# Performance work log

Hardware: AMD Instinct MI355X
Metric: run time of the kernel (lower is better)

Reference implementation:

```python
import jax, jax.numpy as jnp
import numpy as np

HIDDEN = 768
ENT = 9
D = 64  # inner_dim
BIG = 1e12


def _rope_tables(seq_len, dim):
    # layout after torch stack([sin,cos],-1).reshape: [sin0,cos0,sin1,cos1,...]
    pos = jnp.arange(seq_len, dtype=jnp.float32)[:, None]          # [S,1]
    inv = jnp.power(10000.0, -2.0 * jnp.arange(dim // 2, dtype=jnp.float32) / dim)
    ang = pos * inv                                                 # [S,D/2]
    # repeat_interleave(2): [c0,c0,c1,c1,...]
    cos = jnp.repeat(jnp.cos(ang), 2, axis=-1)[:, None, :]          # [S,1,D]
    sin = jnp.repeat(jnp.sin(ang), 2, axis=-1)[:, None, :]
    return sin, cos


def _rotate_half_interleaved(x):
    # stack([-x_odd, x_even], -1).reshape -> [-x1, x0, -x3, x2, ...]
    return jnp.stack([-x[..., 1::2], x[..., ::2]], axis=-1).reshape(x.shape)


def _multilabel_ce(logits, labels):
    # standard GlobalPointer multilabel categorical crossentropy
    B = logits.shape[0]
    y_pred = logits.reshape(B * ENT, -1)
    y_true = labels.reshape(B * ENT, -1)
    y_pred = (1.0 - 2.0 * y_true) * y_pred
    y_neg = y_pred - y_true * BIG
    y_pos = y_pred - (1.0 - y_true) * BIG
    neg = jnp.logaddexp(0.0, jax.scipy.special.logsumexp(y_neg, axis=-1))
    pos = jnp.logaddexp(0.0, jax.scipy.special.logsumexp(y_pos, axis=-1))
    return jnp.mean(neg + pos)


def setup_inputs() -> dict:
    key = jax.random.key(0)
    k1, k2, k3, k4 = jax.random.split(key, 4)
    B, S = 16, 512
    last_hidden_state = jax.random.normal(k1, (B, S, HIDDEN), dtype=jnp.float32)
    attention_mask = jnp.ones((B, S), dtype=jnp.int32)
    batch_labels = jax.random.randint(k2, (B, ENT, S, S), 0, 2).astype(jnp.int32)
    W = jax.random.normal(k3, (HIDDEN, ENT * D * 2), dtype=jnp.float32) * 0.02
    b = jnp.zeros((ENT * D * 2,), dtype=jnp.float32)
    return {"last_hidden_state": last_hidden_state, "attention_mask": attention_mask,
            "batch_labels": batch_labels, "W": W, "b": b}


def reference(last_hidden_state, attention_mask, batch_labels, W, b):
    B, S, _ = last_hidden_state.shape
    out = last_hidden_state @ W + b                     # [B,S,ENT*2D]
    out = out.reshape(B, S, ENT, 2 * D)
    qw, kw = out[..., :D], out[..., D:]                 # [B,S,ENT,D]

    sin, cos = _rope_tables(S, D)                       # [S,1,D]
    qw = qw * cos + _rotate_half_interleaved(qw) * sin
    kw = kw * cos + _rotate_half_interleaved(kw) * sin

    logits = jnp.einsum('bmhd,bnhd->bhmn', qw, kw)      # [B,ENT,S,S]

    pad = attention_mask.astype(jnp.float32)[:, None, None, :]  # mask over key dim n
    logits = logits * pad - (1.0 - pad) * BIG
    tril = jnp.tril(jnp.ones((S, S), dtype=jnp.float32), -1)
    logits = logits - tril * BIG
    temp_logits = logits / (D ** 0.5)

    loss = _multilabel_ce(temp_logits, batch_labels.astype(jnp.float32))
    return loss, temp_logits
```

## Files before the change

kernel.cpp:

```cpp
#include <hip/hip_runtime.h>
#include <hip/hip_bf16.h>

#define HID 768
#define ENTS 9
#define DD 64
#define NOUT 1152
#define BATCH 16
#define SEQ 512
#define BIGF 1000000000000.0f
#define BIG8 125000000000.0f
#define NCHUNK 16

typedef __attribute__((ext_vector_type(8))) short short8;
typedef __attribute__((ext_vector_type(4))) short short4_t;
typedef __attribute__((ext_vector_type(4))) float floatx4;
typedef __attribute__((ext_vector_type(2))) float floatx2;
typedef __attribute__((ext_vector_type(4))) int intx4;
typedef unsigned short ushort_t;

static __device__ __forceinline__ ushort_t f2bf(float x) {
    unsigned int u = __float_as_uint(x);
    unsigned int r = (u + 0x7FFFu + ((u >> 16) & 1u)) >> 16;
    return (ushort_t)r;
}

static __device__ __forceinline__ void gload16(const void* g, void* l) {
    __builtin_amdgcn_global_load_lds(
        (const __attribute__((address_space(1))) void*)g,
        (__attribute__((address_space(3))) void*)l, 16, 0, 0);
}

__global__ __launch_bounds__(256) void prep_kernel(
    const float* __restrict__ X, const float* __restrict__ W,
    float* __restrict__ sin_t, float* __restrict__ cos_t,
    ushort_t* __restrict__ Xb, ushort_t* __restrict__ Wt)
{
    const int tid = blockIdx.x * 256 + threadIdx.x;
    const int nth = gridDim.x * 256;

    for (int idx = tid; idx < SEQ * 32; idx += nth) {
        int m = idx >> 5, i = idx & 31;
        float inv = powf(10000.0f, -2.0f * (float)i / 64.0f);
        float ang = (float)m * inv;
        sin_t[idx] = sinf(ang);
        cos_t[idx] = cosf(ang);
    }
    for (int idx = tid; idx < NOUT * HID; idx += nth) {
        int n = idx / HID, k = idx - n * HID;
        Wt[idx] = f2bf(W[(size_t)k * NOUT + n]);
    }
    const int nx4 = BATCH * SEQ * HID / 4;
    for (int idx = tid; idx < nx4; idx += nth) {
        float4 f = *(const float4*)&X[idx * 4];
        ushort_t* p = &Xb[idx * 4];
        p[0] = f2bf(f.x); p[1] = f2bf(f.y); p[2] = f2bf(f.z); p[3] = f2bf(f.w);
    }
}

__global__ __launch_bounds__(256) void proj_rope_kernel(
    const ushort_t* __restrict__ Xb, const ushort_t* __restrict__ Wt,
    const float* __restrict__ bias,
    const float* __restrict__ sin_t, const float* __restrict__ cos_t,
    ushort_t* __restrict__ qbuf, ushort_t* __restrict__ kbuf)
{
    __shared__ ushort_t As[128 * 32];
    __shared__ ushort_t Bs[128 * 32];
    const int tid  = threadIdx.x;
    const int lane = tid & 63;
    const int wave = tid >> 6;
    const int bm = blockIdx.x * 128;
    const int bn = blockIdx.y * 128;
    const int wm = (wave >> 1) * 64;
    const int wn = (wave & 1) * 64;

    floatx4 acc[4][4];
    #pragma unroll
    for (int j = 0; j < 4; ++j)
        #pragma unroll
        for (int i = 0; i < 4; ++i) { floatx4 z = {0.f,0.f,0.f,0.f}; acc[j][i] = z; }

    const int c0 = wave * 64 + lane;
    const int c1 = 256 + wave * 64 + lane;
    const int r0 = c0 >> 2, q0 = (c0 & 3) * 8;
    const int r1 = c1 >> 2, q1 = (c1 & 3) * 8;
    ushort_t* ldsA0 = As + wave * 512;
    ushort_t* ldsA1 = As + 2048 + wave * 512;
    ushort_t* ldsB0 = Bs + wave * 512;
    ushort_t* ldsB1 = Bs + 2048 + wave * 512;

    const int ko = (lane >> 4) * 8;
    const int lr = lane & 15;

    for (int kt = 0; kt < HID; kt += 32) {
        gload16(&Xb[(size_t)(bm + r0) * HID + kt + q0], ldsA0);
        gload16(&Xb[(size_t)(bm + r1) * HID + kt + q1], ldsA1);
        gload16(&Wt[(size_t)(bn + r0) * HID + kt + q0], ldsB0);
        gload16(&Wt[(size_t)(bn + r1) * HID + kt + q1], ldsB1);
        __syncthreads();

        short8 a[4], b[4];
        #pragma unroll
        for (int i = 0; i < 4; ++i) a[i] = *(const short8*)&As[(wm + i*16 + lr) * 32 + ko];
        #pragma unroll
        for (int j = 0; j < 4; ++j) b[j] = *(const short8*)&Bs[(wn + j*16 + lr) * 32 + ko];
        #pragma unroll
        for (int j = 0; j < 4; ++j)
            #pragma unroll
            for (int i = 0; i < 4; ++i)
                acc[j][i] = __builtin_amdgcn_mfma_f32_16x16x32_bf16(b[j], a[i], acc[j][i], 0, 0, 0);
        __syncthreads();
    }

    #pragma unroll
    for (int j = 0; j < 4; ++j) {
        const int n0 = bn + wn + j*16 + (lane >> 4) * 4;
        const int e   = n0 >> 7;
        const int dd0 = n0 & 127;
        const bool isq = dd0 < DD;
        const int d0  = isq ? dd0 : dd0 - DD;
        const float4 bv = *(const float4*)&bias[n0];
        #pragma unroll
        for (int i = 0; i < 4; ++i) {
            const int m = bm + wm + i*16 + lr;
            const int s  = m & (SEQ - 1);
            const int bb = m >> 9;
            const float c0f = cos_t[s*32 + (d0 >> 1)];
            const float s0f = sin_t[s*32 + (d0 >> 1)];
            const float c1f = cos_t[s*32 + (d0 >> 1) + 1];
            const float s1f = sin_t[s*32 + (d0 >> 1) + 1];
            const float v0 = acc[j][i][0] + bv.x;
            const float v1 = acc[j][i][1] + bv.y;
            const float v2 = acc[j][i][2] + bv.z;
            const float v3 = acc[j][i][3] + bv.w;
            const float o0 = v0 * c0f - v1 * s0f;
            const float o1 = v1 * c0f + v0 * s0f;
            const float o2 = v2 * c1f - v3 * s1f;
            const float o3 = v3 * c1f + v2 * s1f;
            short4_t sv = { (short)f2bf(o0), (short)f2bf(o1), (short)f2bf(o2), (short)f2bf(o3) };
            size_t oidx = (((size_t)(bb * ENTS + e) * SEQ) + s) * DD + d0;
            *(short4_t*)&(isq ? qbuf : kbuf)[oidx] = sv;
        }
    }
}

__global__ __launch_bounds__(256) void qk_mask_ce_kernel(
    const ushort_t* __restrict__ qbuf, const ushort_t* __restrict__ kbuf,
    const int* __restrict__ amask, const int* __restrict__ labels,
    float* __restrict__ logits, float* __restrict__ partials)
{
    __shared__ ushort_t Qs[128][72];
    __shared__ ushort_t Ks[128][72];
    __shared__ float ssn[4], ssp[4];
    const int tid  = threadIdx.x;

    const int wrk = (blockIdx.x & 7) * 288 + (blockIdx.x >> 3);
    const int bh = wrk >> 4;
    const int xy = wrk & 15;
    const int bx = xy >> 2, by = xy & 3;
    const int bm = bx * 128;
    const int bn = by * 128;
    const int b  = bh / ENTS;
    const int bhbase = bh << 18;

    if (bx > by) {
        const int c4 = (tid & 31) << 2;
        const int rr = tid >> 5;

        const intx4 pf = *(const intx4*)&amask[(b << 9) + bn + c4];
        floatx4 cv;
        #pragma unroll
        for (int e = 0; e < 4; ++e) cv[e] = (float)pf[e] * BIG8 - 2.0f * BIG8;
        float cvm1 = 0.f;
        if (c4 > 0) {
            const int pfm1 = amask[(b << 9) + bn + c4 - 1];
            cvm1 = (float)pfm1 * BIG8 - 2.0f * BIG8;
        }
        const floatx4 sh = { cvm1, cv.x, cv.y, cv.z };
        const floatx2 h2 = { cv.y, cv.z };

        int cnt = 0;
        for (int pass = 0; pass < 16; ++pass) {
            const int m = bm + pass * 8 + rr;
            const int off = bhbase + (m << 9) + bn + c4;
            const intx4 y4 = *(const intx4*)&labels[off];
            #pragma unroll
            for (int e = 0; e < 4; ++e) cnt += (y4[e] & 1) & pf[e];
            if (c4 == 0) {
                logits[off] = cv.x;
                *(floatx2*)&logits[off + 1] = h2;
            } else {
                *(floatx4*)&logits[off - 1] = sh;
            }
            if (c4 == 124) logits[off + 3] = cv.w;
        }

        #pragma unroll
        for (int o = 32; o > 0; o >>= 1) cnt += __shfl_down(cnt, o);
        if ((tid & 63) == 0) ssn[tid >> 6] = (float)cnt;
        __syncthreads();
        if (tid == 0) {
            float SP = ssn[0] + ssn[1] + ssn[2] + ssn[3];
            floatx2 res = { 0.f, SP };
            *(floatx2*)&partials[(size_t)(bh * NCHUNK + xy) * 2] = res;
        }
        return;
    }

    const int lane = tid & 63;
    const int wave = tid >> 6;
    const int wm = (wave >> 1) * 64;
    const int wn = (wave & 1) * 64;
    const size_t base = (size_t)bh * SEQ * DD;

    const int g  = lane >> 4;
    const int lr = lane & 15;
    const int ko = g * 8;
    const int r0 = bm + wm + lr;
    const int W  = bn + wn;
    const int n00 = W + (g << 2);

    const bool diag = (bx == by);

    intx4 yc[2][4];
    #pragma unroll
    for (int jh = 0; jh < 2; ++jh)
        #pragma unroll
        for (int i = 0; i < 4; ++i)
            yc[jh][i] = *(const intx4*)&labels[bhbase + ((r0 + i*16) << 9) + n00 + jh*16];

    floatx4 pm8[4], pc[4];
    #pragma unroll
    for (int j = 0; j < 4; ++j) {
        const intx4 p4 = *(const intx4*)&amask[(b << 9) + n00 + j*16];
        #pragma unroll
        for (int rg = 0; rg < 4; ++rg) {
            const float pf = (float)p4[rg];
            pm8[j][rg] = pf * 0.125f;
            pc[j][rg]  = (pf - 1.0f) * BIG8;
        }
    }

    {
        const int r  = tid >> 1;
        const int ks = (tid & 1) * 32;
        const ushort_t* gq = &qbuf[base + (size_t)(bm + r) * DD + ks];
        const ushort_t* gk = &kbuf[base + (size_t)(bn + r) * DD + ks];
        #pragma unroll
        for (int uu = 0; uu < 4; ++uu) {
            *(short8*)&Qs[r][ks + uu*8] = *(const short8*)(gq + uu*8);
            *(short8*)&Ks[r][ks + uu*8] = *(const short8*)(gk + uu*8);
        }
    }
    __syncthreads();

    short8 a[2][4];
    #pragma unroll
    for (int kk = 0; kk < 2; ++kk)
        #pragma unroll
        for (int i = 0; i < 4; ++i)
            a[kk][i] = *(const short8*)&Qs[wm + i*16 + lr][kk*32 + ko];

    float smn = 0.f, smp = 0.f;
    float tl[4];
    float* __restrict__ lgb = logits + bhbase;

    #pragma unroll
    for (int jp = 0; jp < 2; ++jp) {
        const int jA = jp * 2, jB = jp * 2 + 1;

        floatx4 accA[4], accB[4];
        #pragma unroll
        for (int i = 0; i < 4; ++i) { floatx4 z = {0.f,0.f,0.f,0.f}; accA[i] = z; accB[i] = z; }
        #pragma unroll
        for (int kk = 0; kk < 2; ++kk) {
            const short8 bfA = *(const short8*)&Ks[wn + jA*16 + lr][kk*32 + ko];
            const short8 bfB = *(const short8*)&Ks[wn + jB*16 + lr][kk*32 + ko];
            #pragma unroll
            for (int i = 0; i < 4; ++i) {
                accA[i] = __builtin_amdgcn_mfma_f32_16x16x32_bf16(bfA, a[kk][i], accA[i], 0, 0, 0);
                accB[i] = __builtin_amdgcn_mfma_f32_16x16x32_bf16(bfB, a[kk][i], accB[i], 0, 0, 0);
            }
        }

        unsigned int yb = 0;
        {
            int cnt = 0;
            #pragma unroll
            for (int jh = 0; jh < 2; ++jh)
                #pragma unroll
                for (int i = 0; i < 4; ++i)
                    #pragma unroll
                    for (int rg = 0; rg < 4; ++rg) {
                        yb |= (unsigned)(yc[jh][i][rg] & 1) << cnt;
                        ++cnt;
                    }
        }

        if (jp == 0) {
            #pragma unroll
            for (int jh = 0; jh < 2; ++jh)
                #pragma unroll
                for (int i = 0; i < 4; ++i)
                    yc[jh][i] = *(const intx4*)&labels[bhbase + ((r0 + i*16) << 9) + n00 + (2 + jh)*16];
        }

        int cnt = 0;
        #pragma unroll
        for (int half = 0; half < 2; ++half) {
            const int j = half ? jB : jA;
            const floatx4 pm = pm8[j], pcj = pc[j];
            const int n0j = W + j*16 + (g << 2);
            #pragma unroll
            for (int i = 0; i < 4; ++i) {
                const int m = r0 + i*16;
                const int d = m - n0j;
                floatx4 v = half ? accB[i] : accA[i];
                #pragma unroll
                for (int rg = 0; rg < 4; ++rg) {
                    float t = fmaf(v[rg], pm[rg], pcj[rg]);
                    if (diag && (d > rg)) t -= BIG8;
                    v[rg] = t;
                    const int yy = (int)((yb >> cnt) & 1u);
                    const float uu = __uint_as_float(__float_as_uint(t) ^ ((unsigned)yy << 31));
                    const float cN = yy ? -BIGF : 0.0f;
                    const float cP = yy ? -BIG8 : -BIGF;
                    smn += __expf(uu + cN);
                    smp += __expf(uu + cP);
                    ++cnt;
                }
                if (half) accB[i] = v; else accA[i] = v;
            }
        }

        #pragma unroll
        for (int i = 0; i < 4; ++i) {
            const floatx4 vA = accA[i], vB = accB[i];
            const int m = r0 + i*16;
            float* __restrict__ row = lgb + (m << 9);
            const float sameA  = __shfl(vA.w, (lane - 16) & 63);
            const float tailA  = __shfl(tl[i], lr + 48);
            const float sameB  = __shfl(vB.w, (lane - 16) & 63);
            const float crossB = __shfl(vA.w, lr + 48);
            const float uA0 = (g == 0) ? tailA  : sameA;
            const float uB0 = (g == 0) ? crossB : sameB;
            if (jp == 0 && g == 0) {
                row[W] = vA.x;
                floatx2 h2 = { vA.y, vA.z };
                *(floatx2*)&row[W + 1] = h2;
            } else {
                floatx4 uA = { uA0, vA.x, vA.y, vA.z };
                *(floatx4*)&row[W + jA*16 + (g << 2) - 1] = uA;
            }
            floatx4 uB = { uB0, vB.x, vB.y, vB.z };
            *(floatx4*)&row[W + jB*16 + (g << 2) - 1] = uB;
            tl[i] = vB.w;
        }
    }

    if (g == 3) {
        #pragma unroll
        for (int i = 0; i < 4; ++i) {
            const int m = r0 + i*16;
            lgb[(m << 9) + W + 63] = tl[i];
        }
    }

    #pragma unroll
    for (int off = 32; off > 0; off >>= 1) {
        smn += __shfl_down(smn, off);
        smp += __shfl_down(smp, off);
    }
    if (lane == 0) { ssn[wave] = smn; ssp[wave] = smp; }
    __syncthreads();
    if (tid == 0) {
        float SN = ssn[0] + ssn[1] + ssn[2] + ssn[3];
        float SP = ssp[0] + ssp[1] + ssp[2] + ssp[3];
        floatx2 res = { SN, SP };
        *(floatx2*)&partials[(size_t)(bh * NCHUNK + xy) * 2] = res;
    }
}

static __device__ __forceinline__ float lae0(float x) {
    return fmaxf(x, 0.f) + log1pf(__expf(-fabsf(x)));
}

__global__ __launch_bounds__(256) void ce_final_kernel(
    const float* __restrict__ partials, float* __restrict__ out)
{
    __shared__ float red[256];
    const int t = threadIdx.x;
    float val = 0.f;
    if (t < BATCH * ENTS) {
        float SN = 0.f, SP = 0.f;
        for (int c = 0; c < NCHUNK; ++c) {
            SN += partials[(size_t)(t * NCHUNK + c) * 2];
            SP += partials[(size_t)(t * NCHUNK + c) * 2 + 1];
        }
        const float neg = log1pf(SN);
        const float pos = lae0(BIG8 + logf(SP));
        val = neg + pos;
    }
    red[t] = val;
    __syncthreads();
    for (int s2 = 128; s2 > 0; s2 >>= 1) {
        if (t < s2) red[t] += red[t + s2];
        __syncthreads();
    }
    if (t == 0) out[0] = red[0] / (float)(BATCH * ENTS);
}

extern "C" void kernel_launch(void* const* d_in, const int* in_sizes, int n_in,
                              void* d_out, int out_size, void* d_ws, size_t ws_size,
                              hipStream_t stream) {
    const float* X      = (const float*)d_in[0];
    const int*   amask  = (const int*)d_in[1];
    const int*   labels = (const int*)d_in[2];
    const float* W      = (const float*)d_in[3];
    const float* bias   = (const float*)d_in[4];

    float* out    = (float*)d_out;
    float* logits = out + 1;

    float* sin_t = (float*)d_ws;
    float* cos_t = sin_t + SEQ * 32;
    ushort_t* Xb   = (ushort_t*)(cos_t + SEQ * 32);
    ushort_t* Wt   = Xb + (size_t)BATCH * SEQ * HID;
    ushort_t* qbuf = Wt + (size_t)NOUT * HID;
    ushort_t* kbuf = qbuf + (size_t)BATCH * ENTS * SEQ * DD;
    float* partials = (float*)(kbuf + (size_t)BATCH * ENTS * SEQ * DD);

    prep_kernel<<<1024, 256, 0, stream>>>(X, W, sin_t, cos_t, Xb, Wt);
    proj_rope_kernel<<<dim3(64, 9), 256, 0, stream>>>(Xb, Wt, bias, sin_t, cos_t, qbuf, kbuf);
    qk_mask_ce_kernel<<<2304, 256, 0, stream>>>(qbuf, kbuf, amask, labels, logits, partials);
    ce_final_kernel<<<1, 256, 0, stream>>>(partials, out);
}
```

Before: 134.2 us.

## Make QK/CE kernel persistent over three tiles with register prefetch of next Q/K

The QK-logits/CE kernel now launches 768 blocks, each processing three consecutive 128x128 tiles. While the current tile computes, the Q/K rows for the next full tile are prefetched into registers and then stored to shared memory at the start of that tile. The work mapping changes from the interleaved blockIdx swizzle to contiguous triples. The per-column mask is now loaded inside the loop instead of being precomputed. This aims to hide global-load latency and amortize launch cost, at the expense of more register pressure (launch_bounds 256,3), an extra barrier per tile, and possibly load imbalance because consecutive tiles mix masked-only and full tiles.

```diff
diff --git a/kernel.cpp b/kernel.cpp
--- a/kernel.cpp
+++ b/kernel.cpp
@@ -143,7 +143,19 @@
     }
 }
 
-__global__ __launch_bounds__(256) void qk_mask_ce_kernel(
+#define IS_FULL(w_) ((((w_) & 15) >> 2) <= (((w_) & 15) & 3))
+#define STAGE(w_) do {                                                          \
+    const int bh_ = (w_) >> 4, xy_ = (w_) & 15;                                 \
+    const size_t base_ = (size_t)bh_ * SEQ * DD;                                \
+    const ushort_t* gq_ = &qbuf[base_ + (size_t)(((xy_ >> 2) * 128) + r) * DD + ks]; \
+    const ushort_t* gk_ = &kbuf[base_ + (size_t)(((xy_ & 3) * 128) + r) * DD + ks];  \
+    S[0] = *(const short8*)(gq_);      S[1] = *(const short8*)(gq_ + 8);        \
+    S[2] = *(const short8*)(gq_ + 16); S[3] = *(const short8*)(gq_ + 24);       \
+    S[4] = *(const short8*)(gk_);      S[5] = *(const short8*)(gk_ + 8);        \
+    S[6] = *(const short8*)(gk_ + 16); S[7] = *(const short8*)(gk_ + 24);       \
+} while (0)
+
+__global__ __launch_bounds__(256, 3) void qk_mask_ce_kernel(
     const ushort_t* __restrict__ qbuf, const ushort_t* __restrict__ kbuf,
     const int* __restrict__ amask, const int* __restrict__ labels,
     float* __restrict__ logits, float* __restrict__ partials)
@@ -152,231 +164,224 @@
     __shared__ ushort_t Ks[128][72];
     __shared__ float ssn[4], ssp[4];
     const int tid  = threadIdx.x;
-
-    const int wrk = (blockIdx.x & 7) * 288 + (blockIdx.x >> 3);
-    const int bh = wrk >> 4;
-    const int xy = wrk & 15;
-    const int bx = xy >> 2, by = xy & 3;
-    const int bm = bx * 128;
-    const int bn = by * 128;
-    const int b  = bh / ENTS;
-    const int bhbase = bh << 18;
-
-    if (bx > by) {
-        const int c4 = (tid & 31) << 2;
-        const int rr = tid >> 5;
-
-        const intx4 pf = *(const intx4*)&amask[(b << 9) + bn + c4];
-        floatx4 cv;
-        #pragma unroll
-        for (int e = 0; e < 4; ++e) cv[e] = (float)pf[e] * BIG8 - 2.0f * BIG8;
-        float cvm1 = 0.f;
-        if (c4 > 0) {
-            const int pfm1 = amask[(b << 9) + bn + c4 - 1];
-            cvm1 = (float)pfm1 * BIG8 - 2.0f * BIG8;
-        }
-        const floatx4 sh = { cvm1, cv.x, cv.y, cv.z };
-        const floatx2 h2 = { cv.y, cv.z };
-
-        int cnt = 0;
-        for (int pass = 0; pass < 16; ++pass) {
-            const int m = bm + pass * 8 + rr;
-            const int off = bhbase + (m << 9) + bn + c4;
-            const intx4 y4 = *(const intx4*)&labels[off];
-            #pragma unroll
-            for (int e = 0; e < 4; ++e) cnt += (y4[e] & 1) & pf[e];
-            if (c4 == 0) {
-                logits[off] = cv.x;
-                *(floatx2*)&logits[off + 1] = h2;
-            } else {
-                *(floatx4*)&logits[off - 1] = sh;
-            }
-            if (c4 == 124) logits[off + 3] = cv.w;
-        }
-
-        #pragma unroll
-        for (int o = 32; o > 0; o >>= 1) cnt += __shfl_down(cnt, o);
-        if ((tid & 63) == 0) ssn[tid >> 6] = (float)cnt;
-        __syncthreads();
-        if (tid == 0) {
-            float SP = ssn[0] + ssn[1] + ssn[2] + ssn[3];
-            floatx2 res = { 0.f, SP };
-            *(floatx2*)&partials[(size_t)(bh * NCHUNK + xy) * 2] = res;
-        }
-        return;
-    }
-
     const int lane = tid & 63;
     const int wave = tid >> 6;
-    const int wm = (wave >> 1) * 64;
-    const int wn = (wave & 1) * 64;
-    const size_t base = (size_t)bh * SEQ * DD;
-
     const int g  = lane >> 4;
     const int lr = lane & 15;
     const int ko = g * 8;
-    const int r0 = bm + wm + lr;
-    const int W  = bn + wn;
-    const int n00 = W + (g << 2);
-
-    const bool diag = (bx == by);
-
-    intx4 yc[2][4];
-    #pragma unroll
-    for (int jh = 0; jh < 2; ++jh)
-        #pragma unroll
-        for (int i = 0; i < 4; ++i)
-            yc[jh][i] = *(const intx4*)&labels[bhbase + ((r0 + i*16) << 9) + n00 + jh*16];
-
-    floatx4 pm8[4], pc[4];
-    #pragma unroll
-    for (int j = 0; j < 4; ++j) {
-        const intx4 p4 = *(const intx4*)&amask[(b << 9) + n00 + j*16];
-        #pragma unroll
-        for (int rg = 0; rg < 4; ++rg) {
-            const float pf = (float)p4[rg];
-            pm8[j][rg] = pf * 0.125f;
-            pc[j][rg]  = (pf - 1.0f) * BIG8;
-        }
-    }
-
-    {
-        const int r  = tid >> 1;
-        const int ks = (tid & 1) * 32;
-        const ushort_t* gq = &qbuf[base + (size_t)(bm + r) * DD + ks];
-        const ushort_t* gk = &kbuf[base + (size_t)(bn + r) * DD + ks];
-        #pragma unroll
-        for (int uu = 0; uu < 4; ++uu) {
-            *(short8*)&Qs[r][ks + uu*8] = *(const short8*)(gq + uu*8);
-            *(short8*)&Ks[r][ks + uu*8] = *(const short8*)(gk + uu*8);
-        }
-    }
-    __syncthreads();
-
-    short8 a[2][4];
-    #pragma unroll
-    for (int kk = 0; kk < 2; ++kk)
-        #pragma unroll
-        for (int i = 0; i < 4; ++i)
-            a[kk][i] = *(const short8*)&Qs[wm + i*16 + lr][kk*32 + ko];
-
-    float smn = 0.f, smp = 0.f;
-    float tl[4];
-    float* __restrict__ lgb = logits + bhbase;
-
-    #pragma unroll
-    for (int jp = 0; jp < 2; ++jp) {
-        const int jA = jp * 2, jB = jp * 2 + 1;
-
-        floatx4 accA[4], accB[4];
-        #pragma unroll
-        for (int i = 0; i < 4; ++i) { floatx4 z = {0.f,0.f,0.f,0.f}; accA[i] = z; accB[i] = z; }
-        #pragma unroll
-        for (int kk = 0; kk < 2; ++kk) {
-            const short8 bfA = *(const short8*)&Ks[wn + jA*16 + lr][kk*32 + ko];
-            const short8 bfB = *(const short8*)&Ks[wn + jB*16 + lr][kk*32 + ko];
-            #pragma unroll
-            for (int i = 0; i < 4; ++i) {
-                accA[i] = __builtin_amdgcn_mfma_f32_16x16x32_bf16(bfA, a[kk][i], accA[i], 0, 0, 0);
-                accB[i] = __builtin_amdgcn_mfma_f32_16x16x32_bf16(bfB, a[kk][i], accB[i], 0, 0, 0);
-            }
-        }
-
-        unsigned int yb = 0;
-        {
+    const int r  = tid >> 1;
+    const int ks = (tid & 1) * 32;
+
+    short8 S[8];
+    const int w0 = blockIdx.x * 3;
+    if (IS_FULL(w0)) STAGE(w0);
+
+    for (int t = 0; t < 3; ++t) {
+        const int w  = w0 + t;
+        const int bh = w >> 4;
+        const int xy = w & 15;
+        const int bx = xy >> 2, by = xy & 3;
+        const int bm = bx * 128, bn = by * 128;
+        const int b  = bh / ENTS;
+        const int bhbase = bh << 18;
+
+        if (t > 0) __syncthreads();
+
+        if (bx > by) {
+            if (t < 2 && IS_FULL(w + 1)) STAGE(w + 1);
+
+            const int c4 = (tid & 31) << 2;
+            const int rr = tid >> 5;
+            const intx4 pf = *(const intx4*)&amask[(b << 9) + bn + c4];
+            floatx4 cv;
+            #pragma unroll
+            for (int e = 0; e < 4; ++e) cv[e] = (float)pf[e] * BIG8 - 2.0f * BIG8;
+            float cvm1 = 0.f;
+            if (c4 > 0) {
+                const int pfm1 = amask[(b << 9) + bn + c4 - 1];
+                cvm1 = (float)pfm1 * BIG8 - 2.0f * BIG8;
+            }
+            const floatx4 sh = { cvm1, cv.x, cv.y, cv.z };
+            const floatx2 h2 = { cv.y, cv.z };
+
             int cnt = 0;
-            #pragma unroll
-            for (int jh = 0; jh < 2; ++jh)
+            for (int pass = 0; pass < 16; ++pass) {
+                const int m = bm + pass * 8 + rr;
+                const int off = bhbase + (m << 9) + bn + c4;
+                const intx4 y4 = *(const intx4*)&labels[off];
                 #pragma unroll
-                for (int i = 0; i < 4; ++i)
+                for (int e = 0; e < 4; ++e) cnt += (y4[e] & 1) & pf[e];
+                if (c4 == 0) {
+                    logits[off] = cv.x;
+                    *(floatx2*)&logits[off + 1] = h2;
+                } else {
+                    *(floatx4*)&logits[off - 1] = sh;
+                }
+                if (c4 == 124) logits[off + 3] = cv.w;
+            }
+
+            #pragma unroll
+            for (int o = 32; o > 0; o >>= 1) cnt += __shfl_down(cnt, o);
+            if ((tid & 63) == 0) ssn[tid >> 6] = (float)cnt;
+            __syncthreads();
+            if (tid == 0) {
+                float SP = ssn[0] + ssn[1] + ssn[2] + ssn[3];
+                floatx2 res = { 0.f, SP };
+                *(floatx2*)&partials[(size_t)(bh * NCHUNK + xy) * 2] = res;
+            }
+            continue;
+        }
+
+        const int wm = (wave >> 1) * 64;
+        const int wn = (wave & 1) * 64;
+        const int r0 = bm + wm + lr;
+        const int W  = bn + wn;
+        const int n00 = W + (g << 2);
+        const bool diag = (bx == by);
+
+        #pragma unroll
+        for (int u = 0; u < 4; ++u) *(short8*)&Qs[r][ks + u*8] = S[u];
+        #pragma unroll
+        for (int u = 0; u < 4; ++u) *(short8*)&Ks[r][ks + u*8] = S[4 + u];
+        __syncthreads();
+
+        intx4 yc[2][4];
+        #pragma unroll
+        for (int jh = 0; jh < 2; ++jh)
+            #pragma unroll
+            for (int i = 0; i < 4; ++i)
+                yc[jh][i] = *(const intx4*)&labels[bhbase + ((r0 + i*16) << 9) + n00 + jh*16];
+
+        short8 a[2][4];
+        #pragma unroll
+        for (int kk = 0; kk < 2; ++kk)
+            #pragma unroll
+            for (int i = 0; i < 4; ++i)
+                a[kk][i] = *(const short8*)&Qs[wm + i*16 + lr][kk*32 + ko];
+
+        if (t < 2 && IS_FULL(w + 1)) STAGE(w + 1);
+
+        float smn = 0.f, smp = 0.f;
+        float tl[4];
+        float* __restrict__ lgb = logits + bhbase;
+
+        #pragma unroll
+        for (int jp = 0; jp < 2; ++jp) {
+            const int jA = jp * 2, jB = jp * 2 + 1;
+
+            floatx4 accA[4], accB[4];
+            #pragma unroll
+            for (int i = 0; i < 4; ++i) { floatx4 z = {0.f,0.f,0.f,0.f}; accA[i] = z; accB[i] = z; }
+            #pragma unroll
+            for (int kk = 0; kk < 2; ++kk) {
+                const short8 bfA = *(const short8*)&Ks[wn + jA*16 + lr][kk*32 + ko];
+                const short8 bfB = *(const short8*)&Ks[wn + jB*16 + lr][kk*32 + ko];
+                #pragma unroll
+                for (int i = 0; i < 4; ++i) {
+                    accA[i] = __builtin_amdgcn_mfma_f32_16x16x32_bf16(bfA, a[kk][i], accA[i], 0, 0, 0);
+                    accB[i] = __builtin_amdgcn_mfma_f32_16x16x32_bf16(bfB, a[kk][i], accB[i], 0, 0, 0);
+                }
+            }
+
+            unsigned int yb = 0;
+            {
+                int cnt = 0;
+                #pragma unroll
+                for (int jh = 0; jh < 2; ++jh)
+                    #pragma unroll
+                    for (int i = 0; i < 4; ++i)
+                        #pragma unroll
+                        for (int rg = 0; rg < 4; ++rg) {
+                            yb |= (unsigned)(yc[jh][i][rg] & 1) << cnt;
+                            ++cnt;
+                        }
+            }
+            if (jp == 0) {
+                #pragma unroll
+                for (int jh = 0; jh < 2; ++jh)
+                    #pragma unroll
+                    for (int i = 0; i < 4; ++i)
+                        yc[jh][i] = *(const intx4*)&labels[bhbase + ((r0 + i*16) << 9) + n00 + (2 + jh)*16];
+            }
+
+            const intx4 p4A = *(const intx4*)&amask[(b << 9) + n00 + jA*16];
+            const intx4 p4B = *(const intx4*)&amask[(b << 9) + n00 + jB*16];
+
+            int cnt = 0;
+            #pragma unroll
+            for (int half = 0; half < 2; ++half) {
+                const int j = half ? jB : jA;
+                const intx4 p4 = half ? p4B : p4A;
+                const int n0j = W + j*16 + (g << 2);
+                #pragma unroll
+                for (int i = 0; i < 4; ++i) {
+                    const int m = r0 + i*16;
+                    const int d = m - n0j;
+                    floatx4 v = half ? accB[i] : accA[i];
                     #pragma unroll
                     for (int rg = 0; rg < 4; ++rg) {
-                        yb |= (unsigned)(yc[jh][i][rg] & 1) << cnt;
+                        const float pf = (float)p4[rg];
+                        float tt = fmaf(v[rg], pf * 0.125f, (pf - 1.0f) * BIG8);
+                        if (diag && (d > rg)) tt -= BIG8;
+                        v[rg] = tt;
+                        const int yy = (int)((yb >> cnt) & 1u);
+                        const float uu = __uint_as_float(__float_as_uint(tt) ^ ((unsigned)yy << 31));
+                        const float cN = yy ? -BIGF : 0.0f;
+                        const float cP = yy ? -BIG8 : -BIGF;
+                        smn += __expf(uu + cN);
+                        smp += __expf(uu + cP);
                         ++cnt;
                     }
-        }
-
-        if (jp == 0) {
-            #pragma unroll
-            for (int jh = 0; jh < 2; ++jh)
-                #pragma unroll
-                for (int i = 0; i < 4; ++i)
-                    yc[jh][i] = *(const intx4*)&labels[bhbase + ((r0 + i*16) << 9) + n00 + (2 + jh)*16];
-        }
-
-        int cnt = 0;
-        #pragma unroll
-        for (int half = 0; half < 2; ++half) {
-            const int j = half ? jB : jA;
-            const floatx4 pm = pm8[j], pcj = pc[j];
-            const int n0j = W + j*16 + (g << 2);
+                    if (half) accB[i] = v; else accA[i] = v;
+                }
+            }
+
+            #pragma unroll
+            for (int i = 0; i < 4; ++i) {
+                const floatx4 vA = accA[i], vB = accB[i];
+                const int m = r0 + i*16;
+                float* __restrict__ row = lgb + (m << 9);
+                const float sameA  = __shfl(vA.w, (lane - 16) & 63);
+                const float tailA  = __shfl(tl[i], lr + 48);
+                const float sameB  = __shfl(vB.w, (lane - 16) & 63);
+                const float crossB = __shfl(vA.w, lr + 48);
+                const float uA0 = (g == 0) ? tailA  : sameA;
+                const float uB0 = (g == 0) ? crossB : sameB;
+                if (jp == 0 && g == 0) {
+                    row[W] = vA.x;
+                    floatx2 h2 = { vA.y, vA.z };
+                    *(floatx2*)&row[W + 1] = h2;
+                } else {
+                    floatx4 uA = { uA0, vA.x, vA.y, vA.z };
+                    *(floatx4*)&row[W + jA*16 + (g << 2) - 1] = uA;
+                }
+                floatx4 uB = { uB0, vB.x, vB.y, vB.z };
+                *(floatx4*)&row[W + jB*16 + (g << 2) - 1] = uB;
+                tl[i] = vB.w;
+            }
+        }
+
+        if (g == 3) {
             #pragma unroll
             for (int i = 0; i < 4; ++i) {
                 const int m = r0 + i*16;
-                const int d = m - n0j;
-                floatx4 v = half ? accB[i] : accA[i];
-                #pragma unroll
-                for (int rg = 0; rg < 4; ++rg) {
-                    float t = fmaf(v[rg], pm[rg], pcj[rg]);
-                    if (diag && (d > rg)) t -= BIG8;
-                    v[rg] = t;
-                    const int yy = (int)((yb >> cnt) & 1u);
-                    const float uu = __uint_as_float(__float_as_uint(t) ^ ((unsigned)yy << 31));
-                    const float cN = yy ? -BIGF : 0.0f;
-                    const float cP = yy ? -BIG8 : -BIGF;
-                    smn += __expf(uu + cN);
-                    smp += __expf(uu + cP);
-                    ++cnt;
-                }
-                if (half) accB[i] = v; else accA[i] = v;
-            }
-        }
-
-        #pragma unroll
-        for (int i = 0; i < 4; ++i) {
-            const floatx4 vA = accA[i], vB = accB[i];
-            const int m = r0 + i*16;
-            float* __restrict__ row = lgb + (m << 9);
-            const float sameA  = __shfl(vA.w, (lane - 16) & 63);
-            const float tailA  = __shfl(tl[i], lr + 48);
-            const float sameB  = __shfl(vB.w, (lane - 16) & 63);
-            const float crossB = __shfl(vA.w, lr + 48);
-            const float uA0 = (g == 0) ? tailA  : sameA;
-            const float uB0 = (g == 0) ? crossB : sameB;
-            if (jp == 0 && g == 0) {
-                row[W] = vA.x;
-                floatx2 h2 = { vA.y, vA.z };
-                *(floatx2*)&row[W + 1] = h2;
-            } else {
-                floatx4 uA = { uA0, vA.x, vA.y, vA.z };
-                *(floatx4*)&row[W + jA*16 + (g << 2) - 1] = uA;
-            }
-            floatx4 uB = { uB0, vB.x, vB.y, vB.z };
-            *(floatx4*)&row[W + jB*16 + (g << 2) - 1] = uB;
-            tl[i] = vB.w;
-        }
-    }
-
-    if (g == 3) {
-        #pragma unroll
-        for (int i = 0; i < 4; ++i) {
-            const int m = r0 + i*16;
-            lgb[(m << 9) + W + 63] = tl[i];
-        }
-    }
-
-    #pragma unroll
-    for (int off = 32; off > 0; off >>= 1) {
-        smn += __shfl_down(smn, off);
-        smp += __shfl_down(smp, off);
-    }
-    if (lane == 0) { ssn[wave] = smn; ssp[wave] = smp; }
-    __syncthreads();
-    if (tid == 0) {
-        float SN = ssn[0] + ssn[1] + ssn[2] + ssn[3];
-        float SP = ssp[0] + ssp[1] + ssp[2] + ssp[3];
-        floatx2 res = { SN, SP };
-        *(floatx2*)&partials[(size_t)(bh * NCHUNK + xy) * 2] = res;
+                lgb[(m << 9) + W + 63] = tl[i];
+            }
+        }
+
+        #pragma unroll
+        for (int off = 32; off > 0; off >>= 1) {
+            smn += __shfl_down(smn, off);
+            smp += __shfl_down(smp, off);
+        }
+        if (lane == 0) { ssn[wave] = smn; ssp[wave] = smp; }
+        __syncthreads();
+        if (tid == 0) {
+            float SN = ssn[0] + ssn[1] + ssn[2] + ssn[3];
+            float SP = ssp[0] + ssp[1] + ssp[2] + ssp[3];
+            floatx2 res = { SN, SP };
+            *(floatx2*)&partials[(size_t)(bh * NCHUNK + xy) * 2] = res;
+        }
     }
 }
 
@@ -431,6 +436,6 @@
 
     prep_kernel<<<1024, 256, 0, stream>>>(X, W, sin_t, cos_t, Xb, Wt);
     proj_rope_kernel<<<dim3(64, 9), 256, 0, stream>>>(Xb, Wt, bias, sin_t, cos_t, qbuf, kbuf);
-    qk_mask_ce_kernel<<<2304, 256, 0, stream>>>(qbuf, kbuf, amask, labels, logits, partials);
+    qk_mask_ce_kernel<<<768, 256, 0, stream>>>(qbuf, kbuf, amask, labels, logits, partials);
     ce_final_kernel<<<1, 256, 0, stream>>>(partials, out);
 }
```

After: 242.1 us. 1.8x slower.
